# Performance work log

Measured on AMD Instinct MI355X. Metric: run time of the kernel, lower is better.

## Reference

```python
import jax, jax.numpy as jnp
import numpy as np

KH, KW = 3, 3
KN = KH * KW  # kernel_n = 9


def _grid_offset(H, W):
    # Faithful to TF build(): stack(meshgrid(ij)).reshape(-1, 2) -- note this
    # interleaves i- and j- grids in an unusual layout; we replicate it exactly.
    init = jnp.stack(jnp.meshgrid(jnp.arange(KH), jnp.arange(KW), indexing='ij'))
    init = init.reshape(-1, 2).astype(jnp.float32)  # (KN, 2)
    ph, pw = (KH - 1) // 2, (KW - 1) // 2
    g = jnp.stack(
        jnp.meshgrid(jnp.arange(-ph, H - ph), jnp.arange(-pw, W - pw), indexing='ij'),
        axis=-1,
    ).astype(jnp.float32)  # (H, W, 2)
    return g[:, :, None, :] + init[None, None]  # (H, W, KN, 2)


def _bilinear_sample(x, coords):
    # x: (B, H, W, C); coords: (B, H, W, KN, 2) with (row, col) float coords.
    B = x.shape[0]
    y, xc = coords[..., 0], coords[..., 1]
    y0 = jnp.floor(y).astype(jnp.int32)
    y1 = jnp.ceil(y).astype(jnp.int32)   # ceil (not floor+1), faithful to TF code
    x0 = jnp.floor(xc).astype(jnp.int32)
    x1 = jnp.ceil(xc).astype(jnp.int32)
    bidx = jnp.arange(B)[:, None, None, None]

    def g(yy, xx):
        return x[bidx, yy, xx]  # (B, H, W, KN, C)

    v_lt = g(y0, x0)
    v_rb = g(y1, x1)
    v_lb = g(y0, x1)  # (lt_row, rb_col) per TF coords_lb
    v_rt = g(y1, x0)  # (rb_row, lt_col) per TF coords_rt
    fy = (y - y0.astype(y.dtype))[..., None]
    fx = (xc - x0.astype(xc.dtype))[..., None]
    v_t = v_lt + (v_rt - v_lt) * fy
    v_b = v_lb + (v_rb - v_lb) * fy
    return v_t + (v_b - v_t) * fx  # (B, H, W, KN, C)


def setup_inputs() -> dict:
    key = jax.random.key(0)
    k1, k2, k3 = jax.random.split(key, 3)
    B, H, W, C, F = 8, 64, 64, 128, 128
    x = jax.random.normal(k1, (B, H, W, C), dtype=jnp.float32)
    offset = jax.random.normal(k2, (B, H, W, 2 * KN), dtype=jnp.float32)
    Wk = jax.random.truncated_normal(k3, -2.0, 2.0, (KN, C, F), dtype=jnp.float32) * 0.02
    b = jnp.zeros((F,), dtype=jnp.float32)
    return {"x": x, "offset": offset, "W": Wk, "b": b}


def reference(x, offset, W, b):
    B, H, Wd, C = x.shape
    coords = _grid_offset(H, Wd)[None] + offset.reshape(B, H, Wd, KN, 2)
    coords = jnp.stack(
        [
            jnp.clip(coords[..., 0], 0.0, float(H - 1)),
            jnp.clip(coords[..., 1], 0.0, float(Wd - 1)),
        ],
        axis=-1,
    )
    deform = _bilinear_sample(x, coords)  # (B, H, W, KN, C)
    # conv3d with (1,1,KN,C,F) filter, VALID == contraction over (KN, C)
    out = jnp.einsum('bhwnc,ncf->bhwf', deform, W) + b
    return out
```

## Files before the change

### kernel.cpp

```cpp
#include <hip/hip_runtime.h>
#include <stdint.h>

#define KN 9
#define HH 64
#define WW 64
#define CC 128
#define FF 128
#define TM 64
#define NT 512
#define LDK 136

typedef __bf16 bf16x8 __attribute__((ext_vector_type(8)));
typedef float f32x4 __attribute__((ext_vector_type(4)));
typedef unsigned short us8 __attribute__((ext_vector_type(8)));
typedef unsigned short us4 __attribute__((ext_vector_type(4)));

__constant__ float c_init_i[KN] = {0.f,0.f,1.f,2.f,2.f,1.f,0.f,2.f,1.f};
__constant__ float c_init_j[KN] = {0.f,1.f,1.f,2.f,0.f,2.f,1.f,0.f,2.f};

static __device__ inline unsigned short f2bf(float f) {
    union { float f; unsigned u; } v; v.f = f;
    unsigned r = v.u + 0x7fffu + ((v.u >> 16) & 1u);
    return (unsigned short)(r >> 16);
}

__global__ void wt_kernel(const float* __restrict__ Wk, unsigned short* __restrict__ Wt) {
    int idx = blockIdx.x * 256 + threadIdx.x;
    if (idx >= KN * CC * FF) return;
    int n = idx >> 14;
    int rem = idx & 16383;
    int c = rem >> 7;
    int f = rem & 127;
    Wt[(n << 14) + (f << 7) + c] = f2bf(Wk[idx]);
}

__launch_bounds__(NT, 4)
__global__ void deform_kernel(const float* __restrict__ xin,
                              const float* __restrict__ off,
                              const unsigned short* __restrict__ Wt,
                              const float* __restrict__ bias,
                              float* __restrict__ out) {
    __shared__ unsigned short As[TM][LDK];
    __shared__ unsigned short Bt[FF][LDK];
    __shared__ float cY[TM][KN];
    __shared__ float cX[TM][KN];

    const int tid = threadIdx.x;
    const int bb   = blockIdx.x & 7;
    const int hh   = blockIdx.x >> 3;
    const int pix0 = (bb << 12) + (hh << 6);

    for (int t = tid; t < TM * KN; t += NT) {
        int p = t & (TM - 1);
        int n = t >> 6;
        const float* op = off + (size_t)(pix0 + p) * (2 * KN) + 2 * n;
        float y = (float)(hh - 1) + c_init_i[n] + op[0];
        float x = (float)(p - 1) + c_init_j[n] + op[1];
        y = fminf(fmaxf(y, 0.f), 63.f);
        x = fminf(fmaxf(x, 0.f), 63.f);
        cY[p][n] = y;
        cX[p][n] = x;
    }
    __syncthreads();

    const int wave = tid >> 6;
    const int lane = tid & 63;
    const int quad = lane >> 4;
    const int col  = lane & 15;
    const int mt   = wave & 3;
    const int nt0  = (wave >> 2) * 4;

    f32x4 acc[4];
#pragma unroll
    for (int t = 0; t < 4; ++t) acc[t] = (f32x4){0.f, 0.f, 0.f, 0.f};

    const float* bbase = xin + ((size_t)bb << 19);

    for (int n = 0; n < KN; ++n) {
        const unsigned short* Wn = Wt + n * (CC * FF);
        for (int i = tid; i < (FF * CC) / 8; i += NT) {
            int f = i >> 4;
            int o = (i & 15) * 8;
            *(us8*)&Bt[f][o] = *(const us8*)(Wn + f * CC + o);
        }
        for (int i = tid; i < TM * (CC / 4); i += NT) {
            int p  = i >> 5;
            int cg = (i & 31) * 4;
            float y = cY[p][n], x = cX[p][n];
            float fy0 = floorf(y), fx0 = floorf(x);
            int y0 = (int)fy0, x0 = (int)fx0;
            int y1 = (int)ceilf(y), x1 = (int)ceilf(x);
            float fy = y - fy0, fx = x - fx0;
            const float4 vlt = *(const float4*)(bbase + ((((y0 << 6) + x0) << 7) + cg));
            const float4 vrt = *(const float4*)(bbase + ((((y1 << 6) + x0) << 7) + cg));
            const float4 vlb = *(const float4*)(bbase + ((((y0 << 6) + x1) << 7) + cg));
            const float4 vrb = *(const float4*)(bbase + ((((y1 << 6) + x1) << 7) + cg));
            float r0, r1, r2, r3;
            { float vt = vlt.x + (vrt.x - vlt.x) * fy; float vb = vlb.x + (vrb.x - vlb.x) * fy; r0 = vt + (vb - vt) * fx; }
            { float vt = vlt.y + (vrt.y - vlt.y) * fy; float vb = vlb.y + (vrb.y - vlb.y) * fy; r1 = vt + (vb - vt) * fx; }
            { float vt = vlt.z + (vrt.z - vlt.z) * fy; float vb = vlb.z + (vrb.z - vlb.z) * fy; r2 = vt + (vb - vt) * fx; }
            { float vt = vlt.w + (vrt.w - vlt.w) * fy; float vb = vlb.w + (vrb.w - vlb.w) * fy; r3 = vt + (vb - vt) * fx; }
            us4 pk;
            pk.x = f2bf(r0); pk.y = f2bf(r1); pk.z = f2bf(r2); pk.w = f2bf(r3);
            *(us4*)&As[p][cg] = pk;
        }
        __syncthreads();

        const unsigned short* arow = &As[mt * 16 + col][0];
#pragma unroll
        for (int ks = 0; ks < 4; ++ks) {
            bf16x8 a = __builtin_bit_cast(bf16x8, *(const us8*)(arow + ks * 32 + quad * 8));
#pragma unroll
            for (int t = 0; t < 4; ++t) {
                bf16x8 b = __builtin_bit_cast(bf16x8,
                    *(const us8*)(&Bt[(nt0 + t) * 16 + col][ks * 32 + quad * 8]));
                acc[t] = __builtin_amdgcn_mfma_f32_16x16x32_bf16(a, b, acc[t], 0, 0, 0);
            }
        }
        __syncthreads();
    }

#pragma unroll
    for (int t = 0; t < 4; ++t) {
        int f = (nt0 + t) * 16 + col;
        float bv = bias[f];
#pragma unroll
        for (int r = 0; r < 4; ++r) {
            int pr = pix0 + mt * 16 + quad * 4 + r;
            out[(size_t)pr * FF + f] = acc[t][r] + bv;
        }
    }
}

extern "C" void kernel_launch(void* const* d_in, const int* in_sizes, int n_in,
                              void* d_out, int out_size, void* d_ws, size_t ws_size,
                              hipStream_t stream) {
    const float* x    = (const float*)d_in[0];
    const float* off  = (const float*)d_in[1];
    const float* Wk   = (const float*)d_in[2];
    const float* bias = (const float*)d_in[3];
    float* out = (float*)d_out;
    unsigned short* Wt = (unsigned short*)d_ws;

    wt_kernel<<<(KN * CC * FF + 255) / 256, 256, 0, stream>>>(Wk, Wt);
    deform_kernel<<<(8 * HH * WW) / TM, NT, 0, stream>>>(x, off, Wt, bias, out);
}
```

Before: 111.8 us.

## Prefetch next tap's gathers and weights into registers, retile MFMA to 2x2, transpose via LDS

The main loop now issues the bilinear-corner global loads and the weight-slice loads for the next kernel tap into registers before running the current tap's MFMAs, so memory latency overlaps with matrix math. Each wave now computes a 32x32 output tile as 2x2 16x16 MFMAs instead of 16x64, which cuts LDS fragment loads per MFMA. The weight transpose kernel is rewritten to stage through a padded shared-memory tile so its global writes are coalesced. The prefetch registers (about 64 floats plus 4 us8 per thread) raise register pressure, which could lower occupancy under the 512-thread, 4-blocks-per-CU launch bound.

```diff
diff --git a/kernel.cpp b/kernel.cpp
--- a/kernel.cpp
+++ b/kernel.cpp
@@ -25,13 +25,24 @@
 }
 
 __global__ void wt_kernel(const float* __restrict__ Wk, unsigned short* __restrict__ Wt) {
-    int idx = blockIdx.x * 256 + threadIdx.x;
-    if (idx >= KN * CC * FF) return;
-    int n = idx >> 14;
-    int rem = idx & 16383;
-    int c = rem >> 7;
-    int f = rem & 127;
-    Wt[(n << 14) + (f << 7) + c] = f2bf(Wk[idx]);
+    __shared__ unsigned short t[32][33];
+    const int tid = threadIdx.x;
+    const int n  = blockIdx.x >> 4;
+    const int tf = blockIdx.x & 3;
+    const int tc = (blockIdx.x >> 2) & 3;
+    const int g  = tid >> 5;
+    const int l  = tid & 31;
+#pragma unroll
+    for (int r = 0; r < 4; ++r) {
+        int cl = g * 4 + r;
+        t[cl][l] = f2bf(Wk[(n << 14) + ((tc * 32 + cl) << 7) + (tf * 32 + l)]);
+    }
+    __syncthreads();
+#pragma unroll
+    for (int r = 0; r < 4; ++r) {
+        int fl = g * 4 + r;
+        Wt[(n << 14) + ((tf * 32 + fl) << 7) + (tc * 32 + l)] = t[l][fl];
+    }
 }
 
 __launch_bounds__(NT, 4)
@@ -56,10 +67,8 @@
         const float* op = off + (size_t)(pix0 + p) * (2 * KN) + 2 * n;
         float y = (float)(hh - 1) + c_init_i[n] + op[0];
         float x = (float)(p - 1) + c_init_j[n] + op[1];
-        y = fminf(fmaxf(y, 0.f), 63.f);
-        x = fminf(fmaxf(x, 0.f), 63.f);
-        cY[p][n] = y;
-        cX[p][n] = x;
+        cY[p][n] = fminf(fmaxf(y, 0.f), 63.f);
+        cX[p][n] = fminf(fmaxf(x, 0.f), 63.f);
     }
     __syncthreads();
 
@@ -67,67 +76,106 @@
     const int lane = tid & 63;
     const int quad = lane >> 4;
     const int col  = lane & 15;
-    const int mt   = wave & 3;
-    const int nt0  = (wave >> 2) * 4;
+    const int mtile = (wave & 1) * 32;
+    const int ntile = (wave >> 1) * 32;
 
-    f32x4 acc[4];
+    f32x4 acc[2][2];
 #pragma unroll
-    for (int t = 0; t < 4; ++t) acc[t] = (f32x4){0.f, 0.f, 0.f, 0.f};
+    for (int a = 0; a < 2; ++a)
+#pragma unroll
+        for (int b = 0; b < 2; ++b) acc[a][b] = (f32x4){0.f, 0.f, 0.f, 0.f};
 
     const float* bbase = xin + ((size_t)bb << 19);
 
+    auto issue_gather = [&](int n, int k, float4* pf) {
+        int i  = tid + k * NT;
+        int p  = i >> 5;
+        int cg = (i & 31) * 4;
+        float y = cY[p][n], x = cX[p][n];
+        int y0 = (int)floorf(y), x0 = (int)floorf(x);
+        int y1 = (int)ceilf(y),  x1 = (int)ceilf(x);
+        pf[0] = *(const float4*)(bbase + ((((y0 << 6) + x0) << 7) + cg));
+        pf[1] = *(const float4*)(bbase + ((((y1 << 6) + x0) << 7) + cg));
+        pf[2] = *(const float4*)(bbase + ((((y0 << 6) + x1) << 7) + cg));
+        pf[3] = *(const float4*)(bbase + ((((y1 << 6) + x1) << 7) + cg));
+    };
+    auto consume = [&](int n, int k, const float4* pf) {
+        int i  = tid + k * NT;
+        int p  = i >> 5;
+        int cg = (i & 31) * 4;
+        float y = cY[p][n], x = cX[p][n];
+        float fy = y - floorf(y), fx = x - floorf(x);
+        float r0, r1, r2, r3;
+        { float vt = pf[0].x + (pf[1].x - pf[0].x) * fy; float vb = pf[2].x + (pf[3].x - pf[2].x) * fy; r0 = vt + (vb - vt) * fx; }
+        { float vt = pf[0].y + (pf[1].y - pf[0].y) * fy; float vb = pf[2].y + (pf[3].y - pf[2].y) * fy; r1 = vt + (vb - vt) * fx; }
+        { float vt = pf[0].z + (pf[1].z - pf[0].z) * fy; float vb = pf[2].z + (pf[3].z - pf[2].z) * fy; r2 = vt + (vb - vt) * fx; }
+        { float vt = pf[0].w + (pf[1].w - pf[0].w) * fy; float vb = pf[2].w + (pf[3].w - pf[2].w) * fy; r3 = vt + (vb - vt) * fx; }
+        us4 pk;
+        pk.x = f2bf(r0); pk.y = f2bf(r1); pk.z = f2bf(r2); pk.w = f2bf(r3);
+        *(us4*)&As[p][cg] = pk;
+    };
+
+    float4 pf0[4], pf1[4];
+    us8 bpf[4];
+    issue_gather(0, 0, pf0);
+    issue_gather(0, 1, pf1);
+#pragma unroll
+    for (int k = 0; k < 4; ++k) {
+        int i2 = tid + k * NT;
+        bpf[k] = *(const us8*)(Wt + (i2 >> 4) * CC + (i2 & 15) * 8);
+    }
+
     for (int n = 0; n < KN; ++n) {
-        const unsigned short* Wn = Wt + n * (CC * FF);
-        for (int i = tid; i < (FF * CC) / 8; i += NT) {
-            int f = i >> 4;
-            int o = (i & 15) * 8;
-            *(us8*)&Bt[f][o] = *(const us8*)(Wn + f * CC + o);
+        float4 pf2[4], pf3[4];
+        issue_gather(n, 2, pf2);
+        issue_gather(n, 3, pf3);
+#pragma unroll
+        for (int k = 0; k < 4; ++k) {
+            int i2 = tid + k * NT;
+            *(us8*)&Bt[i2 >> 4][(i2 & 15) * 8] = bpf[k];
         }
-        for (int i = tid; i < TM * (CC / 4); i += NT) {
-            int p  = i >> 5;
-            int cg = (i & 31) * 4;
-            float y = cY[p][n], x = cX[p][n];
-            float fy0 = floorf(y), fx0 = floorf(x);
-            int y0 = (int)fy0, x0 = (int)fx0;
-            int y1 = (int)ceilf(y), x1 = (int)ceilf(x);
-            float fy = y - fy0, fx = x - fx0;
-            const float4 vlt = *(const float4*)(bbase + ((((y0 << 6) + x0) << 7) + cg));
-            const float4 vrt = *(const float4*)(bbase + ((((y1 << 6) + x0) << 7) + cg));
-            const float4 vlb = *(const float4*)(bbase + ((((y0 << 6) + x1) << 7) + cg));
-            const float4 vrb = *(const float4*)(bbase + ((((y1 << 6) + x1) << 7) + cg));
-            float r0, r1, r2, r3;
-            { float vt = vlt.x + (vrt.x - vlt.x) * fy; float vb = vlb.x + (vrb.x - vlb.x) * fy; r0 = vt + (vb - vt) * fx; }
-            { float vt = vlt.y + (vrt.y - vlt.y) * fy; float vb = vlb.y + (vrb.y - vlb.y) * fy; r1 = vt + (vb - vt) * fx; }
-            { float vt = vlt.z + (vrt.z - vlt.z) * fy; float vb = vlb.z + (vrb.z - vlb.z) * fy; r2 = vt + (vb - vt) * fx; }
-            { float vt = vlt.w + (vrt.w - vlt.w) * fy; float vb = vlb.w + (vrb.w - vlb.w) * fy; r3 = vt + (vb - vt) * fx; }
-            us4 pk;
-            pk.x = f2bf(r0); pk.y = f2bf(r1); pk.z = f2bf(r2); pk.w = f2bf(r3);
-            *(us4*)&As[p][cg] = pk;
-        }
+        consume(n, 0, pf0);
+        consume(n, 1, pf1);
+        consume(n, 2, pf2);
+        consume(n, 3, pf3);
         __syncthreads();
 
-        const unsigned short* arow = &As[mt * 16 + col][0];
+        if (n + 1 < KN) {
+            issue_gather(n + 1, 0, pf0);
+            issue_gather(n + 1, 1, pf1);
+            const unsigned short* Wn = Wt + (n + 1) * (CC * FF);
+#pragma unroll
+            for (int k = 0; k < 4; ++k) {
+                int i2 = tid + k * NT;
+                bpf[k] = *(const us8*)(Wn + (i2 >> 4) * CC + (i2 & 15) * 8);
+            }
+        }
+
 #pragma unroll
         for (int ks = 0; ks < 4; ++ks) {
-            bf16x8 a = __builtin_bit_cast(bf16x8, *(const us8*)(arow + ks * 32 + quad * 8));
-#pragma unroll
-            for (int t = 0; t < 4; ++t) {
-                bf16x8 b = __builtin_bit_cast(bf16x8,
-                    *(const us8*)(&Bt[(nt0 + t) * 16 + col][ks * 32 + quad * 8]));
-                acc[t] = __builtin_amdgcn_mfma_f32_16x16x32_bf16(a, b, acc[t], 0, 0, 0);
-            }
+            bf16x8 a0 = __builtin_bit_cast(bf16x8, *(const us8*)(&As[mtile + col][ks * 32 + quad * 8]));
+            bf16x8 a1 = __builtin_bit_cast(bf16x8, *(const us8*)(&As[mtile + 16 + col][ks * 32 + quad * 8]));
+            bf16x8 b0 = __builtin_bit_cast(bf16x8, *(const us8*)(&Bt[ntile + col][ks * 32 + quad * 8]));
+            bf16x8 b1 = __builtin_bit_cast(bf16x8, *(const us8*)(&Bt[ntile + 16 + col][ks * 32 + quad * 8]));
+            acc[0][0] = __builtin_amdgcn_mfma_f32_16x16x32_bf16(a0, b0, acc[0][0], 0, 0, 0);
+            acc[0][1] = __builtin_amdgcn_mfma_f32_16x16x32_bf16(a0, b1, acc[0][1], 0, 0, 0);
+            acc[1][0] = __builtin_amdgcn_mfma_f32_16x16x32_bf16(a1, b0, acc[1][0], 0, 0, 0);
+            acc[1][1] = __builtin_amdgcn_mfma_f32_16x16x32_bf16(a1, b1, acc[1][1], 0, 0, 0);
         }
         __syncthreads();
     }
 
 #pragma unroll
-    for (int t = 0; t < 4; ++t) {
-        int f = (nt0 + t) * 16 + col;
+    for (int b = 0; b < 2; ++b) {
+        int f = ntile + b * 16 + col;
         float bv = bias[f];
 #pragma unroll
-        for (int r = 0; r < 4; ++r) {
-            int pr = pix0 + mt * 16 + quad * 4 + r;
-            out[(size_t)pr * FF + f] = acc[t][r] + bv;
+        for (int a = 0; a < 2; ++a) {
+#pragma unroll
+            for (int r = 0; r < 4; ++r) {
+                int pr = pix0 + mtile + a * 16 + quad * 4 + r;
+                out[(size_t)pr * FF + f] = acc[a][b][r] + bv;
+            }
         }
     }
 }
@@ -142,6 +190,6 @@
     float* out = (float*)d_out;
     unsigned short* Wt = (unsigned short*)d_ws;
 
-    wt_kernel<<<(KN * CC * FF + 255) / 256, 256, 0, stream>>>(Wk, Wt);
+    wt_kernel<<<KN * 16, 256, 0, stream>>>(Wk, Wt);
     deform_kernel<<<(8 * HH * WW) / TM, NT, 0, stream>>>(x, off, Wt, bias, out);
 }
```

Result: faster. 104.9 us (-6.2%).
